# Kernel tuning notes

Hardware: AMD Instinct MI355X
Metric: run time of the kernel (lower is better)

## Reference

```python
import jax, jax.numpy as jnp
import numpy as np

GS = 128          # r_group_size
Q_MAX = 7.0       # 2**(q_bits-1)-1, q_bits=4
R_MAX = 7.0       # 2**(r_bits-1)-1, r_bits=4
R_MIN = -8.0      # -R_MAX-1
EPS = 1e-8


def _fake_quant_group(w, n_bits=4, group_size=128, eps=1e-8):
    # symmetric group-wise fake quant of the weight (done once at __init__)
    qmax = 2 ** (n_bits - 1) - 1
    qmin = -qmax - 1
    O, I = w.shape
    wg = w.reshape(O, I // group_size, group_size)
    scale = jnp.maximum(jnp.max(jnp.abs(wg), axis=-1, keepdims=True) / qmax, eps)
    wq = jnp.clip(jnp.round(wg / scale), qmin, qmax) * scale
    return wq.reshape(O, I)


def _select_pow2_base(t):
    # smallest value in {2,4,8,16,32,64} that is >= t (64 if none)
    base = jnp.full_like(t, 64.0)
    for v in (32.0, 16.0, 8.0, 4.0, 2.0):
        base = jnp.where(t <= v, jnp.full_like(t, v), base)
    return base


def setup_inputs() -> dict:
    key = jax.random.key(0)
    kx, kw, kb = jax.random.split(key, 3)
    B, S, IN, OUT = 4, 2048, 4096, 11008
    x = jax.random.normal(kx, (B, S, IN), dtype=jnp.float32)
    w_raw = jax.random.normal(kw, (OUT, IN), dtype=jnp.float32)
    weight = _fake_quant_group(w_raw, n_bits=4, group_size=128)
    bias = jax.random.normal(kb, (OUT,), dtype=jnp.float32)
    return {"x": x, "weight": weight, "bias": bias}


def reference(x, weight, bias):
    # dynamic quotient-remainder activation fake-quant (init path)
    H = x.shape[-1]
    xg = x.astype(jnp.float32).reshape(x.shape[:-1] + (H // GS, GS))  # [..., G, gs]
    max_abs = jnp.maximum(jnp.max(jnp.abs(xg), axis=-1, keepdims=True), EPS)
    base = _select_pow2_base(max_abs / Q_MAX)                 # [..., G, 1]
    q = jnp.clip(jnp.round(xg / base), -Q_MAX, Q_MAX)          # quotient
    r = xg - base * q                                          # remainder
    max_abs_r = jnp.maximum(jnp.max(jnp.abs(r), axis=-1, keepdims=True), EPS)
    scale_r = max_abs_r / R_MAX
    r_dq = jnp.clip(jnp.round(r / scale_r), R_MIN, R_MAX) * scale_r
    x_recon = (base * q + r_dq).reshape(x.shape)
    # F.linear: y = x @ W^T + b
    return jnp.einsum("bsi,oi->bso", x_recon, weight) + bias
```

## Files before the change

### kernel.cpp

```cpp
#include <hip/hip_runtime.h>
#include <stdint.h>
#include <stddef.h>

typedef __bf16 bf16x8 __attribute__((ext_vector_type(8)));
typedef float  f32x4  __attribute__((ext_vector_type(4)));
typedef float  f32x2  __attribute__((ext_vector_type(2)));

__device__ __forceinline__ unsigned short f2bf(float f) {
  unsigned int u = __builtin_bit_cast(unsigned int, f);
  u += 0x7fffu + ((u >> 16) & 1u);
  return (unsigned short)(u >> 16);
}

__device__ __forceinline__ void gld_lds16(const void* g, void* l) {
  __builtin_amdgcn_global_load_lds(
      (__attribute__((address_space(1))) void*)(g),
      (__attribute__((address_space(3))) void*)(l), 16, 0, 0);
}

#define BAR()     asm volatile("s_barrier" ::: "memory")
#define WAITVM(n) asm volatile("s_waitcnt vmcnt(" #n ")" ::: "memory")

__global__ __launch_bounds__(256) void quant_x_kernel(
    const float* __restrict__ x, unsigned short* __restrict__ xb, long long ngroups)
{
  const int lane = threadIdx.x & 63;
  const int wv   = threadIdx.x >> 6;
  long long g = (long long)blockIdx.x * 4 + wv;
  if (g >= ngroups) return;

  const float* xg = x + g * 128;
  f32x2 v = __builtin_nontemporal_load(
      reinterpret_cast<const f32x2*>(xg + lane * 2));

  float m = fmaxf(fabsf(v[0]), fabsf(v[1]));
  #pragma unroll
  for (int off = 32; off; off >>= 1) m = fmaxf(m, __shfl_xor(m, off));
  m = fmaxf(m, 1e-8f);

  float t = m / 7.0f;
  float base = t <= 2.f ? 2.f : t <= 4.f ? 4.f : t <= 8.f ? 8.f
             : t <= 16.f ? 16.f : t <= 32.f ? 32.f : 64.f;
  float inv_base = 1.0f / base;

  float q0 = fminf(fmaxf(rintf(v[0] * inv_base), -7.f), 7.f);
  float q1 = fminf(fmaxf(rintf(v[1] * inv_base), -7.f), 7.f);
  float r0 = v[0] - base * q0;
  float r1 = v[1] - base * q1;

  float mr = fmaxf(fabsf(r0), fabsf(r1));
  #pragma unroll
  for (int off = 32; off; off >>= 1) mr = fmaxf(mr, __shfl_xor(mr, off));
  mr = fmaxf(mr, 1e-8f);
  float scale_r = mr / 7.0f;

  float rd0 = fminf(fmaxf(rintf(r0 / scale_r), -8.f), 7.f) * scale_r;
  float rd1 = fminf(fmaxf(rintf(r1 / scale_r), -8.f), 7.f) * scale_r;

  float y0 = base * q0 + rd0;
  float y1 = base * q1 + rd1;

  unsigned int packed = (unsigned int)f2bf(y0) | ((unsigned int)f2bf(y1) << 16);
  *reinterpret_cast<unsigned int*>(xb + g * 128 + lane * 2) = packed;
}

__global__ __launch_bounds__(256) void cvt_w_kernel(
    const float* __restrict__ w, unsigned short* __restrict__ wb, long long n)
{
  long long i = ((long long)blockIdx.x * blockDim.x + threadIdx.x) * 8;
  if (i + 7 >= n) {
    if (i >= n) return;
    for (long long j = i; j < n; ++j) wb[j] = f2bf(w[j]);
    return;
  }
  f32x4 v0 = __builtin_nontemporal_load(reinterpret_cast<const f32x4*>(w + i));
  f32x4 v1 = __builtin_nontemporal_load(reinterpret_cast<const f32x4*>(w + i + 4));
  uint4 o;
  o.x = (unsigned)f2bf(v0[0]) | ((unsigned)f2bf(v0[1]) << 16);
  o.y = (unsigned)f2bf(v0[2]) | ((unsigned)f2bf(v0[3]) << 16);
  o.z = (unsigned)f2bf(v1[0]) | ((unsigned)f2bf(v1[1]) << 16);
  o.w = (unsigned)f2bf(v1[2]) | ((unsigned)f2bf(v1[3]) << 16);
  *reinterpret_cast<uint4*>(wb + i) = o;
}

#define BM 256
#define BN 256
#define BK 64

#define MFMA16(a, b, c) __builtin_amdgcn_mfma_f32_16x16x32_bf16(a, b, c, 0, 0, 0)

__global__ __launch_bounds__(512, 2) void gemm256_bias(
    const unsigned short* __restrict__ A,
    const unsigned short* __restrict__ B,
    const float* __restrict__ bias,
    float* __restrict__ C,
    int M, int N, int K)
{
  __shared__ unsigned short lds[2][2][2][128 * 64];

  const int tid  = threadIdx.x;
  const int lane = tid & 63;
  const int wid  = tid >> 6;
  const int wm   = wid >> 2;
  const int wn   = wid & 3;
  const int laneq = lane & 15;
  const int laneh = lane >> 4;
  const int lq7   = laneq & 7;

  const int ntm = M / BM;
  const int ntn = N / BN;
  int tm, tn;
  if ((ntm & 15) == 0) {
    int rem = blockIdx.x;
    int str = 0, stc = 0, w = 16;
    for (;;) {
      int w2 = (ntn - stc * 16 < 16) ? (ntn - stc * 16) : 16;
      int sz = 16 * w2;
      if (rem < sz) { w = w2; break; }
      rem -= sz;
      ++stc;
      if (stc * 16 >= ntn) { stc = 0; ++str; }
    }
    tm = str * 16 + rem / w;
    tn = stc * 16 + rem % w;
  } else {
    tm = (int)blockIdx.x / ntn;
    tn = (int)blockIdx.x % ntn;
  }
  const size_t m0 = (size_t)tm * BM;
  const size_t n0 = (size_t)tn * BN;

  const int NT = K / BK;

  const int s0 = ((0 * 4 + laneh) ^ lq7) * 8;
  const int s1 = ((1 * 4 + laneh) ^ lq7) * 8;

  f32x4 acc[8][4];
  #pragma unroll
  for (int i = 0; i < 8; i++)
    #pragma unroll
    for (int j = 0; j < 4; j++)
      acc[i][j] = (f32x4){0.f, 0.f, 0.f, 0.f};

  auto stage = [&](int mat, int d, int h, int kt) {
    const unsigned short* gbase = (mat == 0)
        ? (A + (m0 + (size_t)h * 128) * (size_t)K)
        : (B + (n0 + (size_t)h * 128) * (size_t)K);
    const int k0 = kt * BK;
    #pragma unroll
    for (int l = 0; l < 2; ++l) {
      int c   = l * 512 + tid;
      int row = c >> 3;
      int s   = (c & 7) ^ (row & 7);
      gld_lds16(gbase + (size_t)row * K + k0 + s * 8,
                (char*)&lds[d][mat][h][0] + (l * 512 + wid * 64) * 16);
    }
  };

  stage(0, 0, 0, 0); stage(0, 0, 1, 0);
  stage(1, 0, 0, 0); stage(1, 0, 1, 0);

  for (int t = 0; t < NT; ++t) {
    const int d = t & 1;

    BAR();
    if (t + 1 < NT) {
      const int dn = d ^ 1;
      stage(0, dn, 0, t + 1); stage(0, dn, 1, t + 1);
      stage(1, dn, 0, t + 1); stage(1, dn, 1, t + 1);
      WAITVM(8);
    } else {
      WAITVM(0);
    }
    BAR();

    const unsigned short* As_ = &lds[d][0][wm][0];
    const unsigned short* Bs_ = &lds[d][1][wn >> 1][0];
    const int brow = (wn & 1) * 64;

    bf16x8 al[4][2], ah[4][2], bl[2][2], bh[2][2];

    #pragma unroll
    for (int mi = 0; mi < 4; ++mi) {
      al[mi][0] = *(const bf16x8*)&As_[(mi * 16 + laneq) * 64 + s0];
      al[mi][1] = *(const bf16x8*)&As_[(mi * 16 + laneq) * 64 + s1];
    }
    #pragma unroll
    for (int nj = 0; nj < 2; ++nj) {
      bl[nj][0] = *(const bf16x8*)&Bs_[(brow + nj * 16 + laneq) * 64 + s0];
      bl[nj][1] = *(const bf16x8*)&Bs_[(brow + nj * 16 + laneq) * 64 + s1];
    }
    #pragma unroll
    for (int mi = 0; mi < 4; ++mi)
      #pragma unroll
      for (int nj = 0; nj < 2; ++nj) {
        acc[mi][nj] = MFMA16(al[mi][0], bl[nj][0], acc[mi][nj]);
        acc[mi][nj] = MFMA16(al[mi][1], bl[nj][1], acc[mi][nj]);
      }

    #pragma unroll
    for (int nj = 0; nj < 2; ++nj) {
      bh[nj][0] = *(const bf16x8*)&Bs_[(brow + 32 + nj * 16 + laneq) * 64 + s0];
      bh[nj][1] = *(const bf16x8*)&Bs_[(brow + 32 + nj * 16 + laneq) * 64 + s1];
    }
    #pragma unroll
    for (int mi = 0; mi < 4; ++mi)
      #pragma unroll
      for (int nj = 0; nj < 2; ++nj) {
        acc[mi][2 + nj] = MFMA16(al[mi][0], bh[nj][0], acc[mi][2 + nj]);
        acc[mi][2 + nj] = MFMA16(al[mi][1], bh[nj][1], acc[mi][2 + nj]);
      }

    #pragma unroll
    for (int mi = 0; mi < 4; ++mi) {
      ah[mi][0] = *(const bf16x8*)&As_[(64 + mi * 16 + laneq) * 64 + s0];
      ah[mi][1] = *(const bf16x8*)&As_[(64 + mi * 16 + laneq) * 64 + s1];
    }
    #pragma unroll
    for (int mi = 0; mi < 4; ++mi)
      #pragma unroll
      for (int nj = 0; nj < 2; ++nj) {
        acc[4 + mi][2 + nj] = MFMA16(ah[mi][0], bh[nj][0], acc[4 + mi][2 + nj]);
        acc[4 + mi][2 + nj] = MFMA16(ah[mi][1], bh[nj][1], acc[4 + mi][2 + nj]);
      }
    #pragma unroll
    for (int mi = 0; mi < 4; ++mi)
      #pragma unroll
      for (int nj = 0; nj < 2; ++nj) {
        acc[4 + mi][nj] = MFMA16(ah[mi][0], bl[nj][0], acc[4 + mi][nj]);
        acc[4 + mi][nj] = MFMA16(ah[mi][1], bl[nj][1], acc[4 + mi][nj]);
      }
  }

  #pragma unroll
  for (int nj = 0; nj < 4; ++nj) {
    int col = (int)n0 + wn * 64 + nj * 16 + laneq;
    float bv = bias[col];
    #pragma unroll
    for (int mi = 0; mi < 8; ++mi) {
      size_t row = m0 + wm * 128 + mi * 16 + laneh * 4;
      float* cp = C + row * (size_t)N + col;
      #pragma unroll
      for (int r = 0; r < 4; ++r)
        __builtin_nontemporal_store(acc[mi][nj][r] + bv, cp + (size_t)r * N);
    }
  }
}

extern "C" void kernel_launch(void* const* d_in, const int* in_sizes, int n_in,
                              void* d_out, int out_size, void* d_ws, size_t ws_size,
                              hipStream_t stream) {
  const float* x    = (const float*)d_in[0];
  const float* w    = (const float*)d_in[1];
  const float* bias = (const float*)d_in[2];
  float* out = (float*)d_out;

  const long long xN = in_sizes[0];
  const long long wN = in_sizes[1];
  const int N = in_sizes[2];
  const int K = (int)(wN / N);
  const int M = (int)(xN / K);

  unsigned short* xb = (unsigned short*)d_ws;
  unsigned short* wb = xb + xN;

  long long ngroups = xN / 128;
  long long qblocks = (ngroups + 3) / 4;
  quant_x_kernel<<<(int)qblocks, 256, 0, stream>>>(x, xb, ngroups);

  long long cblocks = (wN + 2047) / 2048;
  cvt_w_kernel<<<(int)cblocks, 256, 0, stream>>>(w, wb, wN);

  int grid = (M / BM) * (N / BN);
  gemm256_bias<<<grid, 512, 0, stream>>>(xb, wb, bias, out, M, N, K);
}
```

Baseline: 803.4 us.

## Deepen GEMM prefetch to two tiles ahead with interleaved staging and priority hints

The bf16 GEMM main loop now issues global-to-LDS loads two K-tiles ahead instead of one. The B and A halves of the next-next tile are staged between MFMA phases, once each half's LDS data has been read into registers. Global and LDS addresses are precomputed as byte offsets, and each MFMA burst is wrapped in s_setprio with sched barriers and lgkmcnt waits. The aim is to hide global load latency and cut address arithmetic, at the cost of more barriers per iteration and more delicate waitcnt bookkeeping.

```diff
diff --git a/kernel.cpp b/kernel.cpp
--- a/kernel.cpp
+++ b/kernel.cpp
@@ -20,6 +20,8 @@
 
 #define BAR()     asm volatile("s_barrier" ::: "memory")
 #define WAITVM(n) asm volatile("s_waitcnt vmcnt(" #n ")" ::: "memory")
+#define WAITLG0() asm volatile("s_waitcnt lgkmcnt(0)" ::: "memory")
+#define SCHED0()  __builtin_amdgcn_sched_barrier(0)
 
 __global__ __launch_bounds__(256) void quant_x_kernel(
     const float* __restrict__ x, unsigned short* __restrict__ xb, long long ngroups)
@@ -132,8 +134,24 @@
 
   const int NT = K / BK;
 
-  const int s0 = ((0 * 4 + laneh) ^ lq7) * 8;
-  const int s1 = ((1 * 4 + laneh) ^ lq7) * 8;
+  const int ss0 = (laneh ^ lq7);
+  const int ss1 = ((4 + laneh) ^ lq7);
+
+  const char* ldsb = (const char*)&lds[0][0][0][0];
+  const int aOff = wm * 16384 + laneq * 128;
+  const int bOff = 32768 + (wn >> 1) * 16384 + ((wn & 1) * 64 + laneq) * 128;
+
+  const int c0 = tid, c1 = 512 + tid;
+  const int r0 = c0 >> 3, sl0 = (c0 & 7) ^ (r0 & 7);
+  const int r1 = c1 >> 3, sl1 = (c1 & 7) ^ (r1 & 7);
+  const unsigned short* gA0 = A + (m0 + r0) * (size_t)K + sl0 * 8;
+  const unsigned short* gA1 = A + (m0 + r1) * (size_t)K + sl1 * 8;
+  const unsigned short* gB0 = B + (n0 + r0) * (size_t)K + sl0 * 8;
+  const unsigned short* gB1 = B + (n0 + r1) * (size_t)K + sl1 * 8;
+  const size_t hstep = (size_t)128 * K;
+
+  char* dst0 = (char*)ldsb + wid * 1024;
+  char* dst1 = dst0 + 65536;
 
   f32x4 acc[8][4];
   #pragma unroll
@@ -142,54 +160,46 @@
     for (int j = 0; j < 4; j++)
       acc[i][j] = (f32x4){0.f, 0.f, 0.f, 0.f};
 
-  auto stage = [&](int mat, int d, int h, int kt) {
-    const unsigned short* gbase = (mat == 0)
-        ? (A + (m0 + (size_t)h * 128) * (size_t)K)
-        : (B + (n0 + (size_t)h * 128) * (size_t)K);
-    const int k0 = kt * BK;
-    #pragma unroll
-    for (int l = 0; l < 2; ++l) {
-      int c   = l * 512 + tid;
-      int row = c >> 3;
-      int s   = (c & 7) ^ (row & 7);
-      gld_lds16(gbase + (size_t)row * K + k0 + s * 8,
-                (char*)&lds[d][mat][h][0] + (l * 512 + wid * 64) * 16);
-    }
-  };
-
-  stage(0, 0, 0, 0); stage(0, 0, 1, 0);
-  stage(1, 0, 0, 0); stage(1, 0, 1, 0);
+  #define STAGE(mat, h, kt, dstD)                                            \
+    do {                                                                     \
+      const unsigned short* g0_ = (mat == 0) ? gA0 : gB0;                    \
+      const unsigned short* g1_ = (mat == 0) ? gA1 : gB1;                    \
+      gld_lds16(g0_ + (size_t)(h) * hstep + (size_t)(kt) * 64,               \
+                (dstD) + (mat) * 32768 + (h) * 16384);                       \
+      gld_lds16(g1_ + (size_t)(h) * hstep + (size_t)(kt) * 64,               \
+                (dstD) + (mat) * 32768 + (h) * 16384 + 8192);                \
+    } while (0)
+
+  STAGE(0, 0, 0, dst0); STAGE(0, 1, 0, dst0);
+  STAGE(1, 0, 0, dst0); STAGE(1, 1, 0, dst0);
+  STAGE(0, 0, 1, dst1); STAGE(0, 1, 1, dst1);
+  STAGE(1, 0, 1, dst1); STAGE(1, 1, 1, dst1);
+  WAITVM(8);
+  BAR();
+
+  bf16x8 al[4][2], ah[4][2], bl[2][2], bh[2][2];
 
   for (int t = 0; t < NT; ++t) {
     const int d = t & 1;
-
-    BAR();
-    if (t + 1 < NT) {
-      const int dn = d ^ 1;
-      stage(0, dn, 0, t + 1); stage(0, dn, 1, t + 1);
-      stage(1, dn, 0, t + 1); stage(1, dn, 1, t + 1);
-      WAITVM(8);
-    } else {
-      WAITVM(0);
-    }
-    BAR();
-
-    const unsigned short* As_ = &lds[d][0][wm][0];
-    const unsigned short* Bs_ = &lds[d][1][wn >> 1][0];
-    const int brow = (wn & 1) * 64;
-
-    bf16x8 al[4][2], ah[4][2], bl[2][2], bh[2][2];
+    const char* aS0 = ldsb + (d << 16) + aOff + ss0 * 16;
+    const char* aS1 = ldsb + (d << 16) + aOff + ss1 * 16;
+    const char* bS0 = ldsb + (d << 16) + bOff + ss0 * 16;
+    const char* bS1 = ldsb + (d << 16) + bOff + ss1 * 16;
+    char* dstn = d ? dst1 : dst0;
 
     #pragma unroll
     for (int mi = 0; mi < 4; ++mi) {
-      al[mi][0] = *(const bf16x8*)&As_[(mi * 16 + laneq) * 64 + s0];
-      al[mi][1] = *(const bf16x8*)&As_[(mi * 16 + laneq) * 64 + s1];
+      al[mi][0] = *(const bf16x8*)(aS0 + mi * 2048);
+      al[mi][1] = *(const bf16x8*)(aS1 + mi * 2048);
     }
     #pragma unroll
     for (int nj = 0; nj < 2; ++nj) {
-      bl[nj][0] = *(const bf16x8*)&Bs_[(brow + nj * 16 + laneq) * 64 + s0];
-      bl[nj][1] = *(const bf16x8*)&Bs_[(brow + nj * 16 + laneq) * 64 + s1];
-    }
+      bl[nj][0] = *(const bf16x8*)(bS0 + nj * 2048);
+      bl[nj][1] = *(const bf16x8*)(bS1 + nj * 2048);
+    }
+    BAR();
+    WAITLG0(); SCHED0();
+    __builtin_amdgcn_s_setprio(1);
     #pragma unroll
     for (int mi = 0; mi < 4; ++mi)
       #pragma unroll
@@ -197,12 +207,16 @@
         acc[mi][nj] = MFMA16(al[mi][0], bl[nj][0], acc[mi][nj]);
         acc[mi][nj] = MFMA16(al[mi][1], bl[nj][1], acc[mi][nj]);
       }
+    __builtin_amdgcn_s_setprio(0);
 
     #pragma unroll
     for (int nj = 0; nj < 2; ++nj) {
-      bh[nj][0] = *(const bf16x8*)&Bs_[(brow + 32 + nj * 16 + laneq) * 64 + s0];
-      bh[nj][1] = *(const bf16x8*)&Bs_[(brow + 32 + nj * 16 + laneq) * 64 + s1];
-    }
+      bh[nj][0] = *(const bf16x8*)(bS0 + 4096 + nj * 2048);
+      bh[nj][1] = *(const bf16x8*)(bS1 + 4096 + nj * 2048);
+    }
+    BAR();
+    WAITLG0(); SCHED0();
+    __builtin_amdgcn_s_setprio(1);
     #pragma unroll
     for (int mi = 0; mi < 4; ++mi)
       #pragma unroll
@@ -210,12 +224,17 @@
         acc[mi][2 + nj] = MFMA16(al[mi][0], bh[nj][0], acc[mi][2 + nj]);
         acc[mi][2 + nj] = MFMA16(al[mi][1], bh[nj][1], acc[mi][2 + nj]);
       }
+    __builtin_amdgcn_s_setprio(0);
 
     #pragma unroll
     for (int mi = 0; mi < 4; ++mi) {
-      ah[mi][0] = *(const bf16x8*)&As_[(64 + mi * 16 + laneq) * 64 + s0];
-      ah[mi][1] = *(const bf16x8*)&As_[(64 + mi * 16 + laneq) * 64 + s1];
-    }
+      ah[mi][0] = *(const bf16x8*)(aS0 + 8192 + mi * 2048);
+      ah[mi][1] = *(const bf16x8*)(aS1 + 8192 + mi * 2048);
+    }
+    BAR();
+    if (t + 2 < NT) { STAGE(1, 0, t + 2, dstn); STAGE(1, 1, t + 2, dstn); }
+    WAITLG0(); SCHED0();
+    __builtin_amdgcn_s_setprio(1);
     #pragma unroll
     for (int mi = 0; mi < 4; ++mi)
       #pragma unroll
@@ -223,6 +242,12 @@
         acc[4 + mi][2 + nj] = MFMA16(ah[mi][0], bh[nj][0], acc[4 + mi][2 + nj]);
         acc[4 + mi][2 + nj] = MFMA16(ah[mi][1], bh[nj][1], acc[4 + mi][2 + nj]);
       }
+    __builtin_amdgcn_s_setprio(0);
+
+    BAR();
+    if (t + 2 < NT) { STAGE(0, 0, t + 2, dstn); STAGE(0, 1, t + 2, dstn); }
+    SCHED0();
+    __builtin_amdgcn_s_setprio(1);
     #pragma unroll
     for (int mi = 0; mi < 4; ++mi)
       #pragma unroll
@@ -230,7 +255,12 @@
         acc[4 + mi][nj] = MFMA16(ah[mi][0], bl[nj][0], acc[4 + mi][nj]);
         acc[4 + mi][nj] = MFMA16(ah[mi][1], bl[nj][1], acc[4 + mi][nj]);
       }
+    __builtin_amdgcn_s_setprio(0);
+    if (t == NT - 2)      { WAITVM(0); }
+    else if (t < NT - 2)  { WAITVM(8); }
+    BAR();
   }
+  #undef STAGE
 
   #pragma unroll
   for (int nj = 0; nj < 4; ++nj) {
```

New measurement: 782.2 us. 2.6% less time.
